# Kernel tuning notes

Measured on AMD Instinct MI355X. Metric: run time of the kernel, lower is better.

Reference implementation:

```python
import jax, jax.numpy as jnp
import numpy as np

RANK, N, T, S = 8, 64, 64, 64
IN_F, OUT_F = N * T, N * S  # 4096, 4096


def setup_inputs() -> dict:
    key = jax.random.key(0)
    k1, k2, k3, k4 = jax.random.split(key, 4)
    scale = 1.0 / np.sqrt(IN_F)
    x = jax.random.normal(k1, (8, 2048, IN_F), dtype=jnp.float32)
    A = jax.random.normal(k2, (RANK, N, T), dtype=jnp.float32) * scale
    B = jax.random.normal(k3, (RANK, S, N), dtype=jnp.float32) * scale
    bias = jax.random.uniform(k4, (OUT_F,), dtype=jnp.float32, minval=-scale, maxval=scale)
    return {"x": x, "A": A, "B": B, "bias": bias}


def reference(x, A, B, bias):
    # Kronecker-product weight reconstruction: sum over rank b of
    # W[i*S+k, j*N+m] = sum_b A[b,i,j] * B[b,k,m]
    W = jnp.einsum('bij,bkm->ikjm', A, B).reshape(OUT_F, IN_F)
    # F.linear: x @ W.T + bias
    return jnp.einsum('bsi,oi->bso', x, W) + bias
```

## Files before the change

kernel.cpp:

```cpp
#include <hip/hip_runtime.h>
#include <stdint.h>

#define M_DIM 16384
#define N_DIM 4096
#define K_DIM 4096
#define KTILES (K_DIM / 32)

typedef short short8 __attribute__((ext_vector_type(8)));
typedef unsigned short ushort8 __attribute__((ext_vector_type(8)));
typedef float f32x4 __attribute__((ext_vector_type(4)));

__device__ __forceinline__ unsigned short f2b(float f) {
    union { float f; uint32_t u; } v; v.f = f;
    return (unsigned short)((v.u + 0x7FFFu + ((v.u >> 16) & 1u)) >> 16);
}

__device__ __forceinline__ void async_ld16(const void* g, void* l) {
    __builtin_amdgcn_global_load_lds(
        (const __attribute__((address_space(1))) uint32_t*)g,
        (__attribute__((address_space(3))) uint32_t*)l, 16, 0, 0);
}

#define VMCNT(n) asm volatile("s_waitcnt vmcnt(" #n ")" ::: "memory")

__device__ __forceinline__ void build_w_body(
    int bid, int tid,
    const float* __restrict__ A, const float* __restrict__ B,
    unsigned short* __restrict__ W)
{
    size_t idx = ((size_t)bid * 256 + tid) * 8;
    int o = (int)(idx >> 12);
    int c = (int)(idx & 4095);
    int i = o >> 6, k = o & 63;
    int j = c >> 6, m0 = c & 63;

    float acc[8];
#pragma unroll
    for (int t = 0; t < 8; ++t) acc[t] = 0.0f;
#pragma unroll
    for (int b = 0; b < 8; ++b) {
        float a = A[b * 4096 + i * 64 + j];
        const float4* bp = (const float4*)&B[b * 4096 + k * 64 + m0];
        float4 b0 = bp[0], b1 = bp[1];
        acc[0] += a * b0.x; acc[1] += a * b0.y;
        acc[2] += a * b0.z; acc[3] += a * b0.w;
        acc[4] += a * b1.x; acc[5] += a * b1.y;
        acc[6] += a * b1.z; acc[7] += a * b1.w;
    }
    ushort8 r;
#pragma unroll
    for (int t = 0; t < 8; ++t) r[t] = f2b(acc[t]);
    *(ushort8*)&W[idx] = r;
}

__global__ __launch_bounds__(256) void build_w_kernel(
    const float* __restrict__ A, const float* __restrict__ B,
    unsigned short* __restrict__ W)
{
    build_w_body(blockIdx.x, threadIdx.x, A, B, W);
}

__global__ __launch_bounds__(256) void prep_kernel(
    const float* __restrict__ x, unsigned short* __restrict__ xb,
    const float* __restrict__ A, const float* __restrict__ B,
    unsigned short* __restrict__ W)
{
    int bid = blockIdx.x;
    if (bid < 32768) {
        size_t idx = ((size_t)bid * 256 + threadIdx.x) * 8;
        const float4* gp = (const float4*)&x[idx];
        float4 v0 = gp[0], v1 = gp[1];
        ushort8 r;
        r[0] = f2b(v0.x); r[1] = f2b(v0.y); r[2] = f2b(v0.z); r[3] = f2b(v0.w);
        r[4] = f2b(v1.x); r[5] = f2b(v1.y); r[6] = f2b(v1.z); r[7] = f2b(v1.w);
        *(ushort8*)&xb[idx] = r;
    } else {
        build_w_body(bid - 32768, threadIdx.x, A, B, W);
    }
}

__global__ __launch_bounds__(512, 2) void gemm256_kernel(
    const unsigned short* __restrict__ xb,
    const unsigned short* __restrict__ W,
    const float* __restrict__ bias,
    float* __restrict__ out)
{
    __shared__ __align__(16) unsigned short AsB[4][256 * 32];
    __shared__ __align__(16) unsigned short BsB[4][256 * 32];

    const int tid = threadIdx.x;
    const int wave = tid >> 6;
    const int lane = tid & 63;
    const int quad = lane >> 4;
    const int l15 = lane & 15;
    const int wr = wave >> 2;
    const int wc = wave & 3;

    const int wg = ((blockIdx.x & 7) << 7) | (blockIdx.x >> 3);
    const size_t mbase = (size_t)(wg >> 4) * 256;
    const int nbase = (wg & 15) * 256;

    const int arow0 = wr * 128 + l15;
    const int brow0 = wc * 64 + l15;

    f32x4 acc[8][4];
#pragma unroll
    for (int a = 0; a < 8; ++a)
#pragma unroll
        for (int b = 0; b < 4; ++b)
            acc[a][b] = (f32x4){0.0f, 0.0f, 0.0f, 0.0f};

    auto stage_half = [&](int tile, int li) {
        const int slot = tile & 3;
        const int f = li * 512 + tid;
        const int row = f >> 2;
        const int kof = tile * 32 + ((((f & 3) ^ ((row >> 1) & 3))) << 3);
        unsigned short* ab = &AsB[slot][(li * 512 + wave * 64) * 8];
        unsigned short* bb = &BsB[slot][(li * 512 + wave * 64) * 8];
        async_ld16(&xb[(mbase + row) * K_DIM + kof], ab);
        async_ld16(&W[(size_t)(nbase + row) * K_DIM + kof], bb);
    };
    auto frag = [&](const unsigned short* buf, int row) -> short8 {
        return *(const short8*)&buf[row * 32 + ((quad ^ ((row >> 1) & 3)) << 3)];
    };

    stage_half(0, 0); stage_half(0, 1);
    stage_half(1, 0); stage_half(1, 1);
    stage_half(2, 0); stage_half(2, 1);
    VMCNT(8);
    __builtin_amdgcn_s_barrier();
    __builtin_amdgcn_sched_barrier(0);

#pragma unroll 1
    for (int t = 0; t < KTILES; ++t) {
        const unsigned short* As_c = AsB[t & 3];
        const unsigned short* Bs_c = BsB[t & 3];

        short8 af[4], bf[4], ag[4];
#pragma unroll
        for (int mt = 0; mt < 4; ++mt) af[mt] = frag(As_c, arow0 + mt * 16);
#pragma unroll
        for (int nt = 0; nt < 4; ++nt) bf[nt] = frag(Bs_c, brow0 + nt * 16);
#pragma unroll
        for (int mt = 0; mt < 4; ++mt) ag[mt] = frag(As_c, arow0 + 64 + mt * 16);
        if ((t + 3) < KTILES) {
            stage_half(t + 3, 0);
            stage_half(t + 3, 1);
        }

        __builtin_amdgcn_s_setprio(1);
#pragma unroll
        for (int mt = 0; mt < 4; ++mt)
#pragma unroll
            for (int nt = 0; nt < 4; ++nt)
                acc[mt][nt] = __builtin_amdgcn_mfma_f32_16x16x32_bf16(
                    af[mt], bf[nt], acc[mt][nt], 0, 0, 0);
#pragma unroll
        for (int mt = 0; mt < 4; ++mt)
#pragma unroll
            for (int nt = 0; nt < 4; ++nt)
                acc[4 + mt][nt] = __builtin_amdgcn_mfma_f32_16x16x32_bf16(
                    ag[mt], bf[nt], acc[4 + mt][nt], 0, 0, 0);
        __builtin_amdgcn_s_setprio(0);

        __builtin_amdgcn_sched_barrier(0);
        if (t < KTILES - 3)       { VMCNT(8); }
        else if (t == KTILES - 3) { VMCNT(4); }
        else                      { VMCNT(0); }
        __builtin_amdgcn_s_barrier();
        __builtin_amdgcn_sched_barrier(0);
    }

    float bv[4];
#pragma unroll
    for (int nt = 0; nt < 4; ++nt) bv[nt] = bias[nbase + wc * 64 + nt * 16 + l15];
#pragma unroll
    for (int mt = 0; mt < 8; ++mt) {
#pragma unroll
        for (int r = 0; r < 4; ++r) {
            const size_t row = mbase + wr * 128 + mt * 16 + quad * 4 + r;
            float* orow = out + row * N_DIM + nbase + wc * 64 + l15;
#pragma unroll
            for (int nt = 0; nt < 4; ++nt)
                orow[nt * 16] = acc[mt][nt][r] + bv[nt];
        }
    }
}

__global__ __launch_bounds__(256, 2) void gemm128_f32(
    const float* __restrict__ xf,
    const unsigned short* __restrict__ W,
    const float* __restrict__ bias,
    float* __restrict__ out)
{
    __shared__ unsigned short As[128 * 32];
    __shared__ unsigned short Bs[128 * 32];

    const int tid = threadIdx.x;
    const int wave = tid >> 6;
    const int lane = tid & 63;
    const int quad = lane >> 4;
    const int l15 = lane & 15;
    const int wm = (wave >> 1) * 64;
    const int wn = (wave & 1) * 64;
    const size_t mbase = (size_t)blockIdx.y * 128;
    const int nbase = blockIdx.x * 128;

    f32x4 acc[4][4];
#pragma unroll
    for (int a = 0; a < 4; ++a)
#pragma unroll
        for (int b = 0; b < 4; ++b)
            acc[a][b] = (f32x4){0.0f, 0.0f, 0.0f, 0.0f};

    for (int k0 = 0; k0 < K_DIM; k0 += 32) {
        {
            const int issue0 = wave * 2;
#pragma unroll
            for (int t = 0; t < 2; ++t) {
                const int isn = issue0 + t;
                const int row = isn * 16 + (lane >> 2);
                const int kc = (lane & 3) * 8;
                async_ld16(&W[(size_t)(nbase + row) * K_DIM + k0 + kc],
                           &Bs[isn * 512]);
            }
        }
        {
            const int row = tid >> 1;
            const int half = tid & 1;
            const float* gp = xf + (mbase + row) * K_DIM + k0 + half * 16;
            float4 v0 = ((const float4*)gp)[0];
            float4 v1 = ((const float4*)gp)[1];
            float4 v2 = ((const float4*)gp)[2];
            float4 v3 = ((const float4*)gp)[3];
            ushort8 lo, hi;
            lo[0] = f2b(v0.x); lo[1] = f2b(v0.y); lo[2] = f2b(v0.z); lo[3] = f2b(v0.w);
            lo[4] = f2b(v1.x); lo[5] = f2b(v1.y); lo[6] = f2b(v1.z); lo[7] = f2b(v1.w);
            hi[0] = f2b(v2.x); hi[1] = f2b(v2.y); hi[2] = f2b(v2.z); hi[3] = f2b(v2.w);
            hi[4] = f2b(v3.x); hi[5] = f2b(v3.y); hi[6] = f2b(v3.z); hi[7] = f2b(v3.w);
            *(ushort8*)&As[row * 32 + half * 16] = lo;
            *(ushort8*)&As[row * 32 + half * 16 + 8] = hi;
        }
        __syncthreads();

        short8 af[4], bf[4];
#pragma unroll
        for (int mt = 0; mt < 4; ++mt)
            af[mt] = *(const short8*)&As[(wm + mt * 16 + l15) * 32 + quad * 8];
#pragma unroll
        for (int nt = 0; nt < 4; ++nt)
            bf[nt] = *(const short8*)&Bs[(wn + nt * 16 + l15) * 32 + quad * 8];
#pragma unroll
        for (int mt = 0; mt < 4; ++mt)
#pragma unroll
            for (int nt = 0; nt < 4; ++nt)
                acc[mt][nt] = __builtin_amdgcn_mfma_f32_16x16x32_bf16(
                    af[mt], bf[nt], acc[mt][nt], 0, 0, 0);
        __syncthreads();
    }

    float bv[4];
#pragma unroll
    for (int nt = 0; nt < 4; ++nt) bv[nt] = bias[nbase + wn + nt * 16 + l15];
#pragma unroll
    for (int mt = 0; mt < 4; ++mt) {
#pragma unroll
        for (int r = 0; r < 4; ++r) {
            const size_t row = mbase + wm + mt * 16 + quad * 4 + r;
            float* orow = out + row * N_DIM + nbase + wn + l15;
#pragma unroll
            for (int nt = 0; nt < 4; ++nt)
                orow[nt * 16] = acc[mt][nt][r] + bv[nt];
        }
    }
}

extern "C" void kernel_launch(void* const* d_in, const int* in_sizes, int n_in,
                              void* d_out, int out_size, void* d_ws, size_t ws_size,
                              hipStream_t stream)
{
    const float* x = (const float*)d_in[0];
    const float* A = (const float*)d_in[1];
    const float* B = (const float*)d_in[2];
    const float* bias = (const float*)d_in[3];
    float* out = (float*)d_out;

    unsigned short* Wb = (unsigned short*)d_ws;
    const size_t wbytes = (size_t)N_DIM * K_DIM * 2;
    const size_t xbytes = (size_t)M_DIM * K_DIM * 2;

    if (ws_size >= wbytes + xbytes) {
        unsigned short* xbuf = (unsigned short*)((char*)d_ws + wbytes);
        prep_kernel<<<32768 + 8192, 256, 0, stream>>>(x, xbuf, A, B, Wb);
        gemm256_kernel<<<dim3(1024), 512, 0, stream>>>(xbuf, Wb, bias, out);
    } else {
        build_w_kernel<<<(N_DIM * (size_t)K_DIM) / 8 / 256, 256, 0, stream>>>(A, B, Wb);
        gemm128_f32<<<dim3(N_DIM / 128, M_DIM / 128), 256, 0, stream>>>(x, Wb, bias, out);
    }
}
```

Baseline: 951.3 us.

## Prefetch next-tile B fragments in GEMM loop and widen x conversion per thread

The GEMM main loop now reads the B fragments for tile t+1 during tile t and carries them in registers. This requires the next tile's data to be resident earlier, so the vmcnt waits are tightened from 8 to 4 outstanding loads, and the loop is unrolled by two. Separately, the x-to-bf16 prep kernel now converts 16 floats per thread and launches half as many blocks. The aim is to hide LDS read latency for B behind the MFMAs and to cut block-launch overhead in the prep step. The cost is more register pressure and a shallower effective prefetch depth for global loads.

```diff
diff --git a/kernel.cpp b/kernel.cpp
--- a/kernel.cpp
+++ b/kernel.cpp
@@ -66,16 +66,19 @@
     unsigned short* __restrict__ W)
 {
     int bid = blockIdx.x;
-    if (bid < 32768) {
-        size_t idx = ((size_t)bid * 256 + threadIdx.x) * 8;
+    if (bid < 16384) {
+        size_t idx = ((size_t)bid * 256 + threadIdx.x) * 16;
         const float4* gp = (const float4*)&x[idx];
-        float4 v0 = gp[0], v1 = gp[1];
-        ushort8 r;
-        r[0] = f2b(v0.x); r[1] = f2b(v0.y); r[2] = f2b(v0.z); r[3] = f2b(v0.w);
-        r[4] = f2b(v1.x); r[5] = f2b(v1.y); r[6] = f2b(v1.z); r[7] = f2b(v1.w);
-        *(ushort8*)&xb[idx] = r;
+        float4 v0 = gp[0], v1 = gp[1], v2 = gp[2], v3 = gp[3];
+        ushort8 r0, r1;
+        r0[0] = f2b(v0.x); r0[1] = f2b(v0.y); r0[2] = f2b(v0.z); r0[3] = f2b(v0.w);
+        r0[4] = f2b(v1.x); r0[5] = f2b(v1.y); r0[6] = f2b(v1.z); r0[7] = f2b(v1.w);
+        r1[0] = f2b(v2.x); r1[1] = f2b(v2.y); r1[2] = f2b(v2.z); r1[3] = f2b(v2.w);
+        r1[4] = f2b(v3.x); r1[5] = f2b(v3.y); r1[6] = f2b(v3.z); r1[7] = f2b(v3.w);
+        *(ushort8*)&xb[idx] = r0;
+        *(ushort8*)&xb[idx + 8] = r1;
     } else {
-        build_w_body(bid - 32768, threadIdx.x, A, B, W);
+        build_w_body(bid - 16384, threadIdx.x, A, B, W);
     }
 }
 
@@ -127,22 +130,27 @@
     stage_half(0, 0); stage_half(0, 1);
     stage_half(1, 0); stage_half(1, 1);
     stage_half(2, 0); stage_half(2, 1);
-    VMCNT(8);
+    VMCNT(4);
     __builtin_amdgcn_s_barrier();
     __builtin_amdgcn_sched_barrier(0);
 
-#pragma unroll 1
+    short8 bf_cur[4];
+#pragma unroll
+    for (int nt = 0; nt < 4; ++nt) bf_cur[nt] = frag(BsB[0], brow0 + nt * 16);
+
+#pragma unroll 2
     for (int t = 0; t < KTILES; ++t) {
         const unsigned short* As_c = AsB[t & 3];
-        const unsigned short* Bs_c = BsB[t & 3];
-
-        short8 af[4], bf[4], ag[4];
-#pragma unroll
-        for (int mt = 0; mt < 4; ++mt) af[mt] = frag(As_c, arow0 + mt * 16);
-#pragma unroll
-        for (int nt = 0; nt < 4; ++nt) bf[nt] = frag(Bs_c, brow0 + nt * 16);
-#pragma unroll
-        for (int mt = 0; mt < 4; ++mt) ag[mt] = frag(As_c, arow0 + 64 + mt * 16);
+        const unsigned short* Bs_n = BsB[(t + 1) & 3];
+
+        short8 af_lo[4], af_hi[4], bf_nxt[4];
+#pragma unroll
+        for (int mt = 0; mt < 4; ++mt) af_lo[mt] = frag(As_c, arow0 + mt * 16);
+#pragma unroll
+        for (int mt = 0; mt < 4; ++mt) af_hi[mt] = frag(As_c, arow0 + 64 + mt * 16);
+#pragma unroll
+        for (int nt = 0; nt < 4; ++nt) bf_nxt[nt] = frag(Bs_n, brow0 + nt * 16);
+
         if ((t + 3) < KTILES) {
             stage_half(t + 3, 0);
             stage_half(t + 3, 1);
@@ -154,19 +162,20 @@
 #pragma unroll
             for (int nt = 0; nt < 4; ++nt)
                 acc[mt][nt] = __builtin_amdgcn_mfma_f32_16x16x32_bf16(
-                    af[mt], bf[nt], acc[mt][nt], 0, 0, 0);
+                    af_lo[mt], bf_cur[nt], acc[mt][nt], 0, 0, 0);
 #pragma unroll
         for (int mt = 0; mt < 4; ++mt)
 #pragma unroll
             for (int nt = 0; nt < 4; ++nt)
                 acc[4 + mt][nt] = __builtin_amdgcn_mfma_f32_16x16x32_bf16(
-                    ag[mt], bf[nt], acc[4 + mt][nt], 0, 0, 0);
+                    af_hi[mt], bf_cur[nt], acc[4 + mt][nt], 0, 0, 0);
         __builtin_amdgcn_s_setprio(0);
 
+#pragma unroll
+        for (int nt = 0; nt < 4; ++nt) bf_cur[nt] = bf_nxt[nt];
+
         __builtin_amdgcn_sched_barrier(0);
-        if (t < KTILES - 3)       { VMCNT(8); }
-        else if (t == KTILES - 3) { VMCNT(4); }
-        else                      { VMCNT(0); }
+        if (t < KTILES - 3) { VMCNT(4); } else { VMCNT(0); }
         __builtin_amdgcn_s_barrier();
         __builtin_amdgcn_sched_barrier(0);
     }
@@ -291,7 +300,7 @@
 
     if (ws_size >= wbytes + xbytes) {
         unsigned short* xbuf = (unsigned short*)((char*)d_ws + wbytes);
-        prep_kernel<<<32768 + 8192, 256, 0, stream>>>(x, xbuf, A, B, Wb);
+        prep_kernel<<<16384 + 8192, 256, 0, stream>>>(x, xbuf, A, B, Wb);
         gemm256_kernel<<<dim3(1024), 512, 0, stream>>>(xbuf, Wb, bias, out);
     } else {
         build_w_kernel<<<(N_DIM * (size_t)K_DIM) / 8 / 256, 256, 0, stream>>>(A, B, Wb);
```

New measurement: 942.6 us. Within noise of the previous version (-0.9%).
